# Performance work log

Measured on AMD Instinct MI355X. Metric: run time of the kernel, lower is better.

The kernel has to match this reference:

```python
import jax, jax.numpy as jnp
import numpy as np
from jax.ops import segment_sum

N_NODES = 100000
N_EDGES = 1600000
IN_DIM, HID_DIM, OUT_DIM = 64, 48, 32


def setup_inputs() -> dict:
    key = jax.random.key(0)
    ks = jax.random.split(key, 4)
    x = jax.random.normal(ks[0], (N_NODES, IN_DIM), dtype=jnp.float32)
    edge_index = jax.random.randint(ks[1], (2, N_EDGES), 0, N_NODES, dtype=jnp.int64)
    W1 = jax.random.normal(ks[2], (IN_DIM, HID_DIM), dtype=jnp.float32) / np.sqrt(IN_DIM)
    b1 = jnp.zeros((HID_DIM,), dtype=jnp.float32)
    W2 = jax.random.normal(ks[3], (HID_DIM, OUT_DIM), dtype=jnp.float32) / np.sqrt(HID_DIM)
    b2 = jnp.zeros((OUT_DIM,), dtype=jnp.float32)
    return {"x": x, "edge_index": edge_index, "W1": W1, "b1": b1, "W2": W2, "b2": b2}


def _gcn_conv(x, W, b, src, dst, deg_inv_sqrt, n_nodes):
    # GCNConv: out = D^{-1/2} (A + I) D^{-1/2} (x W) + b
    h = x @ W                                   # [N, F_out]
    norm = deg_inv_sqrt[src] * deg_inv_sqrt[dst]  # [E+N]
    msg = h[src] * norm[:, None]                # gather + scale
    out = segment_sum(msg, dst, num_segments=n_nodes)  # scatter-add over dst
    return out + b


def reference(x, edge_index, W1, b1, W2, b2):
    n = x.shape[0]
    loop = jnp.arange(n, dtype=edge_index.dtype)
    src = jnp.concatenate([edge_index[0], loop])  # add self-loops (PyG default)
    dst = jnp.concatenate([edge_index[1], loop])
    deg = segment_sum(jnp.ones_like(dst, dtype=x.dtype), dst, num_segments=n)
    deg_inv_sqrt = jnp.where(deg > 0, jax.lax.rsqrt(jnp.maximum(deg, 1.0)), 0.0)
    h = _gcn_conv(x, W1, b1, src, dst, deg_inv_sqrt, n)
    h = jax.nn.relu(h)
    embeddings = _gcn_conv(h, W2, b2, src, dst, deg_inv_sqrt, n)
    return embeddings
```

## Files before the change

### kernel.cpp

```cpp
#include <hip/hip_runtime.h>
#include <hip/hip_fp16.h>


#define NN 100000
#define NE 1600000
#define NPB 128
#define NBUCK ((NN + NPB - 1) / NPB)
#define PBITS 17
#define PMASK ((1 << PBITS) - 1)
#define CHB 3
#define CHS 14
#define NKEY (NPB << CHB)
#define PART_B 512
#define EPT 8
#define PART_G ((NE + PART_B * EPT - 1) / (PART_B * EPT))
#define CAP 4096
#define UN 8

struct alignas(8)  half4 { __half2 lo, hi; };
struct alignas(16) half8 { __half2 a, b, c, d; };

__global__ void k_part(const int* __restrict__ src, const int* __restrict__ dst,
                       int* __restrict__ cursor, int* __restrict__ packed) {
    __shared__ int h[NBUCK];
    __shared__ int base[NBUCK];
    for (int i = threadIdx.x; i < NBUCK; i += blockDim.x) h[i] = 0;
    __syncthreads();
    int ebase = blockIdx.x * (PART_B * EPT);
    for (int k = 0; k < EPT; ++k) {
        int e = ebase + k * PART_B + threadIdx.x;
        if (e < NE) atomicAdd(&h[dst[e] >> 7], 1);
    }
    __syncthreads();
    for (int i = threadIdx.x; i < NBUCK; i += blockDim.x) {
        int c = h[i];
        if (c) base[i] = atomicAdd(&cursor[i], c);
        h[i] = 0;
    }
    __syncthreads();
    for (int k = 0; k < EPT; ++k) {
        int e = ebase + k * PART_B + threadIdx.x;
        if (e < NE) {
            int d = dst[e];
            int b = d >> 7;
            int r = atomicAdd(&h[b], 1);
            packed[(size_t)b * CAP + base[b] + r] = src[e] | ((d & (NPB - 1)) << PBITS);
        }
    }
}

__global__ void k_bsort(const int* __restrict__ packed, const int* __restrict__ cursor,
                        int* __restrict__ srcsort, unsigned int* __restrict__ rowinfo,
                        float* __restrict__ dinv) {
    __shared__ int stage[CAP];
    __shared__ int cnt[NKEY];
    __shared__ int tsum[256];
    int tid = threadIdx.x, b = blockIdx.x;
    int e0 = b * CAP, sz = cursor[b];
    for (int i = tid; i < NKEY; i += 256) cnt[i] = 0;
    __syncthreads();
    for (int i = tid; i < sz; i += 256) {
        int w = packed[e0 + i];
        stage[i] = w;
        int key = ((w >> PBITS) << CHB) | ((w & PMASK) >> CHS);
        atomicAdd(&cnt[key], 1);
    }
    __syncthreads();
    int k0 = tid * 4;
    int c0 = cnt[k0], c1 = cnt[k0 + 1], c2 = cnt[k0 + 2], c3 = cnt[k0 + 3];
    int loc = c0 + c1 + c2 + c3;
    tsum[tid] = loc;
    __syncthreads();
    for (int off = 1; off < 256; off <<= 1) {
        int v = (tid >= off) ? tsum[tid - off] : 0;
        __syncthreads();
        tsum[tid] += v;
        __syncthreads();
    }
    int base = tsum[tid] - loc;
    cnt[k0]     = base;
    cnt[k0 + 1] = base + c0;
    cnt[k0 + 2] = base + c0 + c1;
    cnt[k0 + 3] = base + c0 + c1 + c2;
    __syncthreads();
    if (tid < NPB) {
        int node = b * NPB + tid;
        int rs = cnt[tid << CHB];
        int re = (tid == NPB - 1) ? sz : cnt[(tid + 1) << CHB];
        if (node < NN) {
            rowinfo[node] = ((unsigned int)(e0 + rs) << 10) | (unsigned int)(re - rs);
            dinv[node] = rsqrtf((float)(re - rs + 1));
        }
    }
    __syncthreads();
    for (int i = tid; i < sz; i += 256) {
        int w = stage[i];
        int key = ((w >> PBITS) << CHB) | ((w & PMASK) >> CHS);
        int p = atomicAdd(&cnt[key], 1);
        srcsort[e0 + p] = w & PMASK;
    }
}

template <int K, int NC, int CPT>
__global__ __launch_bounds__(256) void
k_gemm(const float* __restrict__ X, const float* __restrict__ W,
       const float* __restrict__ dinv, __half* __restrict__ Hh, int M) {
    constexpr int CG = NC / CPT;
    constexpr int MT = (256 / CG) * 2;
    constexpr int KF4 = K / 4;
    __shared__ float w[K * NC];
    int tid = threadIdx.x;
    int R0 = blockIdx.x * MT;
    for (int i = tid; i < K * NC; i += 256) w[i] = W[i];
    __syncthreads();

    int tc = tid % CG, tr = tid / CG;
    int r0 = R0 + 2 * tr, r1 = r0 + 1;
    int c0 = tc * CPT;
    bool ok0 = r0 < M, ok1 = r1 < M;
    const float4* X4 = (const float4*)X;
    const float4 z4 = make_float4(0.f, 0.f, 0.f, 0.f);

    float acc[2][CPT];
#pragma unroll
    for (int rr = 0; rr < 2; ++rr)
#pragma unroll
        for (int j = 0; j < CPT; ++j) acc[rr][j] = 0.f;

#pragma unroll 2
    for (int k4 = 0; k4 < KF4; ++k4) {
        float4 xa = ok0 ? X4[(size_t)r0 * KF4 + k4] : z4;
        float4 xb = ok1 ? X4[(size_t)r1 * KF4 + k4] : z4;
        float ar[4] = {xa.x, xa.y, xa.z, xa.w};
        float br[4] = {xb.x, xb.y, xb.z, xb.w};
#pragma unroll
        for (int j = 0; j < 4; ++j) {
            float va = ar[j], vb = br[j];
#pragma unroll
            for (int q = 0; q < CPT / 4; ++q) {
                float4 wv = *(const float4*)&w[(4 * k4 + j) * NC + c0 + 4 * q];
                acc[0][q*4+0] = fmaf(va, wv.x, acc[0][q*4+0]);
                acc[0][q*4+1] = fmaf(va, wv.y, acc[0][q*4+1]);
                acc[0][q*4+2] = fmaf(va, wv.z, acc[0][q*4+2]);
                acc[0][q*4+3] = fmaf(va, wv.w, acc[0][q*4+3]);
                acc[1][q*4+0] = fmaf(vb, wv.x, acc[1][q*4+0]);
                acc[1][q*4+1] = fmaf(vb, wv.y, acc[1][q*4+1]);
                acc[1][q*4+2] = fmaf(vb, wv.z, acc[1][q*4+2]);
                acc[1][q*4+3] = fmaf(vb, wv.w, acc[1][q*4+3]);
            }
        }
    }
#pragma unroll
    for (int rr = 0; rr < 2; ++rr) {
        int gr = r0 + rr;
        if (gr >= M) continue;
        float d = dinv[gr];
#pragma unroll
        for (int q = 0; q < CPT / 4; ++q) {
            __half2 p0 = __floats2half2_rn(acc[rr][q*4+0] * d, acc[rr][q*4+1] * d);
            __half2 p1 = __floats2half2_rn(acc[rr][q*4+2] * d, acc[rr][q*4+3] * d);
            half4 hv; hv.lo = p0; hv.hi = p1;
            *(half4*)(Hh + (size_t)gr * NC + c0 + 4 * q) = hv;
        }
    }
}

__global__ __launch_bounds__(256) void
k_fused48(const __half* __restrict__ Hh, const unsigned int* __restrict__ rowinfo,
          const int* __restrict__ srcsort, const float* __restrict__ dinv,
          const float* __restrict__ b1, const float* __restrict__ W2,
          __half* __restrict__ Hh2) {
    constexpr int ROWS = 128, XS = 49;
    __shared__ float Xs[ROWS * XS];
    __shared__ float w2[48 * 32];
    __shared__ float bb[48];
    int tid = threadIdx.x;
    int R0 = blockIdx.x * ROWS;
    for (int i = tid; i < 48 * 32; i += 256) w2[i] = W2[i];
    if (tid < 48) bb[tid] = b1[tid];
    __syncthreads();

    for (int t = tid; t < ROWS * 6; t += 256) {
        int lr = t / 6, q = t - lr * 6;
        int r = R0 + lr;
        if (r >= NN) continue;
        half8 sv = *(const half8*)(Hh + (size_t)r * 48 + 8 * q);
        float2 f0 = __half22float2(sv.a), f1 = __half22float2(sv.b);
        float2 f2 = __half22float2(sv.c), f3 = __half22float2(sv.d);
        float a0 = f0.x, a1 = f0.y, a2 = f1.x, a3 = f1.y;
        float a4 = f2.x, a5 = f2.y, a6 = f3.x, a7 = f3.y;
        unsigned int rp = rowinfo[r];
        int e0 = rp >> 10, e1 = e0 + (int)(rp & 1023);
        for (int e = e0; e < e1; e += UN) {
            int ss[UN]; float ms[UN];
#pragma unroll
            for (int u = 0; u < UN; ++u) {
                int ee = e + u;
                bool ok = ee < e1;
                ss[u] = srcsort[ok ? ee : e0];
                ms[u] = ok ? 1.f : 0.f;
            }
            half8 vv[UN];
#pragma unroll
            for (int u = 0; u < UN; ++u)
                vv[u] = *(const half8*)(Hh + (size_t)ss[u] * 48 + 8 * q);
#pragma unroll
            for (int u = 0; u < UN; ++u) {
                float2 g0 = __half22float2(vv[u].a), g1 = __half22float2(vv[u].b);
                float2 g2 = __half22float2(vv[u].c), g3 = __half22float2(vv[u].d);
                float m = ms[u];
                a0 = fmaf(g0.x, m, a0); a1 = fmaf(g0.y, m, a1);
                a2 = fmaf(g1.x, m, a2); a3 = fmaf(g1.y, m, a3);
                a4 = fmaf(g2.x, m, a4); a5 = fmaf(g2.y, m, a5);
                a6 = fmaf(g3.x, m, a6); a7 = fmaf(g3.y, m, a7);
            }
        }
        float d = dinv[r];
        float* xr = &Xs[lr * XS + 8 * q];
        const float* bf = &bb[8 * q];
        xr[0] = fmaxf(fmaf(a0, d, bf[0]), 0.f);
        xr[1] = fmaxf(fmaf(a1, d, bf[1]), 0.f);
        xr[2] = fmaxf(fmaf(a2, d, bf[2]), 0.f);
        xr[3] = fmaxf(fmaf(a3, d, bf[3]), 0.f);
        xr[4] = fmaxf(fmaf(a4, d, bf[4]), 0.f);
        xr[5] = fmaxf(fmaf(a5, d, bf[5]), 0.f);
        xr[6] = fmaxf(fmaf(a6, d, bf[6]), 0.f);
        xr[7] = fmaxf(fmaf(a7, d, bf[7]), 0.f);
    }
    __syncthreads();

    int tc = tid & 3, tr = tid >> 2;
    int r0l = 2 * tr, c0 = tc * 8;
    float acc[2][8];
#pragma unroll
    for (int rr = 0; rr < 2; ++rr)
#pragma unroll
        for (int j = 0; j < 8; ++j) acc[rr][j] = 0.f;
#pragma unroll 4
    for (int k = 0; k < 48; ++k) {
        float x0 = Xs[r0l * XS + k];
        float x1 = Xs[(r0l + 1) * XS + k];
        float4 wv0 = *(const float4*)&w2[k * 32 + c0];
        float4 wv1 = *(const float4*)&w2[k * 32 + c0 + 4];
        acc[0][0] = fmaf(x0, wv0.x, acc[0][0]); acc[0][1] = fmaf(x0, wv0.y, acc[0][1]);
        acc[0][2] = fmaf(x0, wv0.z, acc[0][2]); acc[0][3] = fmaf(x0, wv0.w, acc[0][3]);
        acc[0][4] = fmaf(x0, wv1.x, acc[0][4]); acc[0][5] = fmaf(x0, wv1.y, acc[0][5]);
        acc[0][6] = fmaf(x0, wv1.z, acc[0][6]); acc[0][7] = fmaf(x0, wv1.w, acc[0][7]);
        acc[1][0] = fmaf(x1, wv0.x, acc[1][0]); acc[1][1] = fmaf(x1, wv0.y, acc[1][1]);
        acc[1][2] = fmaf(x1, wv0.z, acc[1][2]); acc[1][3] = fmaf(x1, wv0.w, acc[1][3]);
        acc[1][4] = fmaf(x1, wv1.x, acc[1][4]); acc[1][5] = fmaf(x1, wv1.y, acc[1][5]);
        acc[1][6] = fmaf(x1, wv1.z, acc[1][6]); acc[1][7] = fmaf(x1, wv1.w, acc[1][7]);
    }
#pragma unroll
    for (int rr = 0; rr < 2; ++rr) {
        int gr = R0 + r0l + rr;
        if (gr >= NN) continue;
        float d = dinv[gr];
        __half2 p0 = __floats2half2_rn(acc[rr][0] * d, acc[rr][1] * d);
        __half2 p1 = __floats2half2_rn(acc[rr][2] * d, acc[rr][3] * d);
        __half2 p2 = __floats2half2_rn(acc[rr][4] * d, acc[rr][5] * d);
        __half2 p3 = __floats2half2_rn(acc[rr][6] * d, acc[rr][7] * d);
        half8 hv; hv.a = p0; hv.b = p1; hv.c = p2; hv.d = p3;
        *(half8*)(Hh2 + (size_t)gr * 32 + c0) = hv;
    }
}

template <int NC>
__global__ void k_agg(const __half* __restrict__ Hh, const unsigned int* __restrict__ rowinfo,
                      const int* __restrict__ srcsort, const float* __restrict__ dinv,
                      const float* __restrict__ bias, float* __restrict__ out) {
    constexpr int Q = NC / 8;
    int idx = blockIdx.x * blockDim.x + threadIdx.x;
    if (idx >= NN * Q) return;
    int r = idx / Q, q = idx - r * Q;
    half8 sv = *(const half8*)(Hh + (size_t)r * NC + 8 * q);
    float2 f0 = __half22float2(sv.a), f1 = __half22float2(sv.b);
    float2 f2 = __half22float2(sv.c), f3 = __half22float2(sv.d);
    float a0 = f0.x, a1 = f0.y, a2 = f1.x, a3 = f1.y;
    float a4 = f2.x, a5 = f2.y, a6 = f3.x, a7 = f3.y;
    unsigned int rp = rowinfo[r];
    int e0 = rp >> 10, e1 = e0 + (int)(rp & 1023);
    for (int e = e0; e < e1; e += UN) {
        int ss[UN]; float ms[UN];
#pragma unroll
        for (int u = 0; u < UN; ++u) {
            int ee = e + u;
            bool ok = ee < e1;
            ss[u] = srcsort[ok ? ee : e0];
            ms[u] = ok ? 1.f : 0.f;
        }
        half8 vv[UN];
#pragma unroll
        for (int u = 0; u < UN; ++u)
            vv[u] = *(const half8*)(Hh + (size_t)ss[u] * NC + 8 * q);
#pragma unroll
        for (int u = 0; u < UN; ++u) {
            float2 g0 = __half22float2(vv[u].a), g1 = __half22float2(vv[u].b);
            float2 g2 = __half22float2(vv[u].c), g3 = __half22float2(vv[u].d);
            float m = ms[u];
            a0 = fmaf(g0.x, m, a0); a1 = fmaf(g0.y, m, a1);
            a2 = fmaf(g1.x, m, a2); a3 = fmaf(g1.y, m, a3);
            a4 = fmaf(g2.x, m, a4); a5 = fmaf(g2.y, m, a5);
            a6 = fmaf(g3.x, m, a6); a7 = fmaf(g3.y, m, a7);
        }
    }
    float d = dinv[r];
    const float4* b4 = (const float4*)bias;
    float4 bv0 = b4[2 * q], bv1 = b4[2 * q + 1];
    a0 = fmaf(a0, d, bv0.x); a1 = fmaf(a1, d, bv0.y);
    a2 = fmaf(a2, d, bv0.z); a3 = fmaf(a3, d, bv0.w);
    a4 = fmaf(a4, d, bv1.x); a5 = fmaf(a5, d, bv1.y);
    a6 = fmaf(a6, d, bv1.z); a7 = fmaf(a7, d, bv1.w);
    float4* o4 = (float4*)(out + (size_t)r * NC + 8 * q);
    o4[0] = make_float4(a0, a1, a2, a3);
    o4[1] = make_float4(a4, a5, a6, a7);
}

extern "C" void kernel_launch(void* const* d_in, const int* in_sizes, int n_in,
                              void* d_out, int out_size, void* d_ws, size_t ws_size,
                              hipStream_t stream) {
    const float* x  = (const float*)d_in[0];
    const int*   ei = (const int*)d_in[1];
    const float* W1 = (const float*)d_in[2];
    const float* b1 = (const float*)d_in[3];
    const float* W2 = (const float*)d_in[4];
    const float* b2 = (const float*)d_in[5];
    float* out = (float*)d_out;

    const int* src = ei;
    const int* dst = ei + NE;

    char* p = (char*)d_ws;
    auto take = [&](size_t elems) { void* q = p; p += ((elems * 4 + 255) & ~255ull); return q; };
    int*          cursor  = (int*)take(NBUCK);
    unsigned int* rowinfo = (unsigned int*)take(NN);
    float*        dinv    = (float*)take(NN);
    int*          srcsort = (int*)take((size_t)NBUCK * CAP);
    __half*       Hh      = (__half*)take((size_t)NN * 24);
    int*          packed  = (int*)take((size_t)NBUCK * CAP);
    __half*       Hh2     = (__half*)packed;

    const int B = 256;
    const int GB = (NN + 127) / 128;
    hipMemsetAsync(cursor, 0, NBUCK * sizeof(int), stream);
    k_part<<<PART_G, PART_B, 0, stream>>>(src, dst, cursor, packed);
    k_bsort<<<NBUCK, 256, 0, stream>>>(packed, cursor, srcsort, rowinfo, dinv);

    k_gemm<64, 48, 12><<<GB, 256, 0, stream>>>(x, W1, dinv, Hh, NN);
    k_fused48<<<GB, 256, 0, stream>>>(Hh, rowinfo, srcsort, dinv, b1, W2, Hh2);
    k_agg<32><<<(NN * 4 + B - 1) / B, B, 0, stream>>>(Hh2, rowinfo, srcsort, dinv, b2, out);
}
```

Before: 207.0 us.

## Merge first GEMM with edge partitioning into one launch, move source scaling to gather

The layer-1 GEMM and the edge-partition pass now run in a single kernel, with block indices split between the two jobs, so that independent work overlaps and one launch is removed. Because the GEMM now runs before degrees are known, it no longer multiplies by dinv[src]. The aggregation kernel instead loads dinv for each gathered neighbour and for the self row. This adds one extra random 4-byte gather per edge in the fused layer-1 kernel and enlarges the partition blocks' shared-memory footprint by the W buffer.

```diff
diff --git a/kernel.cpp b/kernel.cpp
--- a/kernel.cpp
+++ b/kernel.cpp
@@ -11,40 +11,98 @@
 #define CHB 3
 #define CHS 14
 #define NKEY (NPB << CHB)
-#define PART_B 512
-#define EPT 8
-#define PART_G ((NE + PART_B * EPT - 1) / (PART_B * EPT))
 #define CAP 4096
 #define UN 8
+#define GEMMB ((NN + 127) / 128)
+#define EPT 8
+#define PARTB ((NE + 2047) / 2048)
 
 struct alignas(8)  half4 { __half2 lo, hi; };
 struct alignas(16) half8 { __half2 a, b, c, d; };
 
-__global__ void k_part(const int* __restrict__ src, const int* __restrict__ dst,
-                       int* __restrict__ cursor, int* __restrict__ packed) {
+__global__ __launch_bounds__(256) void
+k_fat(const float* __restrict__ X, const float* __restrict__ W,
+      __half* __restrict__ Hh,
+      const int* __restrict__ src, const int* __restrict__ dst,
+      int* __restrict__ cursor, int* __restrict__ packed) {
+    __shared__ float w[64 * 48];
     __shared__ int h[NBUCK];
     __shared__ int base[NBUCK];
-    for (int i = threadIdx.x; i < NBUCK; i += blockDim.x) h[i] = 0;
-    __syncthreads();
-    int ebase = blockIdx.x * (PART_B * EPT);
-    for (int k = 0; k < EPT; ++k) {
-        int e = ebase + k * PART_B + threadIdx.x;
-        if (e < NE) atomicAdd(&h[dst[e] >> 7], 1);
-    }
-    __syncthreads();
-    for (int i = threadIdx.x; i < NBUCK; i += blockDim.x) {
-        int c = h[i];
-        if (c) base[i] = atomicAdd(&cursor[i], c);
-        h[i] = 0;
-    }
-    __syncthreads();
-    for (int k = 0; k < EPT; ++k) {
-        int e = ebase + k * PART_B + threadIdx.x;
-        if (e < NE) {
-            int d = dst[e];
-            int b = d >> 7;
-            int r = atomicAdd(&h[b], 1);
-            packed[(size_t)b * CAP + base[b] + r] = src[e] | ((d & (NPB - 1)) << PBITS);
+    int tid = threadIdx.x;
+    if (blockIdx.x < GEMMB) {
+        int R0 = blockIdx.x * 128;
+        for (int i = tid; i < 64 * 48; i += 256) w[i] = W[i];
+        __syncthreads();
+        int tc = tid & 3, tr = tid >> 2;
+        int r0 = R0 + 2 * tr, r1 = r0 + 1;
+        int c0 = tc * 12;
+        bool ok0 = r0 < NN, ok1 = r1 < NN;
+        const float4* X4 = (const float4*)X;
+        const float4 z4 = make_float4(0.f, 0.f, 0.f, 0.f);
+        float acc[2][12];
+#pragma unroll
+        for (int rr = 0; rr < 2; ++rr)
+#pragma unroll
+            for (int j = 0; j < 12; ++j) acc[rr][j] = 0.f;
+#pragma unroll 2
+        for (int k4 = 0; k4 < 16; ++k4) {
+            float4 xa = ok0 ? X4[(size_t)r0 * 16 + k4] : z4;
+            float4 xb = ok1 ? X4[(size_t)r1 * 16 + k4] : z4;
+            float ar[4] = {xa.x, xa.y, xa.z, xa.w};
+            float br[4] = {xb.x, xb.y, xb.z, xb.w};
+#pragma unroll
+            for (int j = 0; j < 4; ++j) {
+                float va = ar[j], vb = br[j];
+#pragma unroll
+                for (int q = 0; q < 3; ++q) {
+                    float4 wv = *(const float4*)&w[(4 * k4 + j) * 48 + c0 + 4 * q];
+                    acc[0][q*4+0] = fmaf(va, wv.x, acc[0][q*4+0]);
+                    acc[0][q*4+1] = fmaf(va, wv.y, acc[0][q*4+1]);
+                    acc[0][q*4+2] = fmaf(va, wv.z, acc[0][q*4+2]);
+                    acc[0][q*4+3] = fmaf(va, wv.w, acc[0][q*4+3]);
+                    acc[1][q*4+0] = fmaf(vb, wv.x, acc[1][q*4+0]);
+                    acc[1][q*4+1] = fmaf(vb, wv.y, acc[1][q*4+1]);
+                    acc[1][q*4+2] = fmaf(vb, wv.z, acc[1][q*4+2]);
+                    acc[1][q*4+3] = fmaf(vb, wv.w, acc[1][q*4+3]);
+                }
+            }
+        }
+#pragma unroll
+        for (int rr = 0; rr < 2; ++rr) {
+            int gr = r0 + rr;
+            if (gr >= NN) continue;
+#pragma unroll
+            for (int q = 0; q < 3; ++q) {
+                __half2 p0 = __floats2half2_rn(acc[rr][q*4+0], acc[rr][q*4+1]);
+                __half2 p1 = __floats2half2_rn(acc[rr][q*4+2], acc[rr][q*4+3]);
+                half4 hv; hv.lo = p0; hv.hi = p1;
+                *(half4*)(Hh + (size_t)gr * 48 + c0 + 4 * q) = hv;
+            }
+        }
+    } else {
+        int pb = blockIdx.x - GEMMB;
+        for (int i = tid; i < NBUCK; i += 256) h[i] = 0;
+        __syncthreads();
+        int ebase = pb * 2048;
+        for (int k = 0; k < EPT; ++k) {
+            int e = ebase + k * 256 + tid;
+            if (e < NE) atomicAdd(&h[dst[e] >> 7], 1);
+        }
+        __syncthreads();
+        for (int i = tid; i < NBUCK; i += 256) {
+            int c = h[i];
+            if (c) base[i] = atomicAdd(&cursor[i], c);
+            h[i] = 0;
+        }
+        __syncthreads();
+        for (int k = 0; k < EPT; ++k) {
+            int e = ebase + k * 256 + tid;
+            if (e < NE) {
+                int d = dst[e];
+                int b = d >> 7;
+                int r = atomicAdd(&h[b], 1);
+                packed[(size_t)b * CAP + base[b] + r] = src[e] | ((d & (NPB - 1)) << PBITS);
+            }
         }
     }
 }
@@ -98,70 +156,6 @@
         int key = ((w >> PBITS) << CHB) | ((w & PMASK) >> CHS);
         int p = atomicAdd(&cnt[key], 1);
         srcsort[e0 + p] = w & PMASK;
-    }
-}
-
-template <int K, int NC, int CPT>
-__global__ __launch_bounds__(256) void
-k_gemm(const float* __restrict__ X, const float* __restrict__ W,
-       const float* __restrict__ dinv, __half* __restrict__ Hh, int M) {
-    constexpr int CG = NC / CPT;
-    constexpr int MT = (256 / CG) * 2;
-    constexpr int KF4 = K / 4;
-    __shared__ float w[K * NC];
-    int tid = threadIdx.x;
-    int R0 = blockIdx.x * MT;
-    for (int i = tid; i < K * NC; i += 256) w[i] = W[i];
-    __syncthreads();
-
-    int tc = tid % CG, tr = tid / CG;
-    int r0 = R0 + 2 * tr, r1 = r0 + 1;
-    int c0 = tc * CPT;
-    bool ok0 = r0 < M, ok1 = r1 < M;
-    const float4* X4 = (const float4*)X;
-    const float4 z4 = make_float4(0.f, 0.f, 0.f, 0.f);
-
-    float acc[2][CPT];
-#pragma unroll
-    for (int rr = 0; rr < 2; ++rr)
-#pragma unroll
-        for (int j = 0; j < CPT; ++j) acc[rr][j] = 0.f;
-
-#pragma unroll 2
-    for (int k4 = 0; k4 < KF4; ++k4) {
-        float4 xa = ok0 ? X4[(size_t)r0 * KF4 + k4] : z4;
-        float4 xb = ok1 ? X4[(size_t)r1 * KF4 + k4] : z4;
-        float ar[4] = {xa.x, xa.y, xa.z, xa.w};
-        float br[4] = {xb.x, xb.y, xb.z, xb.w};
-#pragma unroll
-        for (int j = 0; j < 4; ++j) {
-            float va = ar[j], vb = br[j];
-#pragma unroll
-            for (int q = 0; q < CPT / 4; ++q) {
-                float4 wv = *(const float4*)&w[(4 * k4 + j) * NC + c0 + 4 * q];
-                acc[0][q*4+0] = fmaf(va, wv.x, acc[0][q*4+0]);
-                acc[0][q*4+1] = fmaf(va, wv.y, acc[0][q*4+1]);
-                acc[0][q*4+2] = fmaf(va, wv.z, acc[0][q*4+2]);
-                acc[0][q*4+3] = fmaf(va, wv.w, acc[0][q*4+3]);
-                acc[1][q*4+0] = fmaf(vb, wv.x, acc[1][q*4+0]);
-                acc[1][q*4+1] = fmaf(vb, wv.y, acc[1][q*4+1]);
-                acc[1][q*4+2] = fmaf(vb, wv.z, acc[1][q*4+2]);
-                acc[1][q*4+3] = fmaf(vb, wv.w, acc[1][q*4+3]);
-            }
-        }
-    }
-#pragma unroll
-    for (int rr = 0; rr < 2; ++rr) {
-        int gr = r0 + rr;
-        if (gr >= M) continue;
-        float d = dinv[gr];
-#pragma unroll
-        for (int q = 0; q < CPT / 4; ++q) {
-            __half2 p0 = __floats2half2_rn(acc[rr][q*4+0] * d, acc[rr][q*4+1] * d);
-            __half2 p1 = __floats2half2_rn(acc[rr][q*4+2] * d, acc[rr][q*4+3] * d);
-            half4 hv; hv.lo = p0; hv.hi = p1;
-            *(half4*)(Hh + (size_t)gr * NC + c0 + 4 * q) = hv;
-        }
     }
 }
 
@@ -184,38 +178,40 @@
         int lr = t / 6, q = t - lr * 6;
         int r = R0 + lr;
         if (r >= NN) continue;
+        float d = dinv[r];
         half8 sv = *(const half8*)(Hh + (size_t)r * 48 + 8 * q);
         float2 f0 = __half22float2(sv.a), f1 = __half22float2(sv.b);
         float2 f2 = __half22float2(sv.c), f3 = __half22float2(sv.d);
-        float a0 = f0.x, a1 = f0.y, a2 = f1.x, a3 = f1.y;
-        float a4 = f2.x, a5 = f2.y, a6 = f3.x, a7 = f3.y;
+        float a0 = f0.x * d, a1 = f0.y * d, a2 = f1.x * d, a3 = f1.y * d;
+        float a4 = f2.x * d, a5 = f2.y * d, a6 = f3.x * d, a7 = f3.y * d;
         unsigned int rp = rowinfo[r];
         int e0 = rp >> 10, e1 = e0 + (int)(rp & 1023);
         for (int e = e0; e < e1; e += UN) {
-            int ss[UN]; float ms[UN];
+            int ss[UN]; bool okb[UN];
 #pragma unroll
             for (int u = 0; u < UN; ++u) {
                 int ee = e + u;
-                bool ok = ee < e1;
-                ss[u] = srcsort[ok ? ee : e0];
-                ms[u] = ok ? 1.f : 0.f;
-            }
+                okb[u] = ee < e1;
+                ss[u] = srcsort[okb[u] ? ee : e0];
+            }
+            float dd[UN];
+#pragma unroll
+            for (int u = 0; u < UN; ++u) dd[u] = dinv[ss[u]];
             half8 vv[UN];
 #pragma unroll
             for (int u = 0; u < UN; ++u)
                 vv[u] = *(const half8*)(Hh + (size_t)ss[u] * 48 + 8 * q);
 #pragma unroll
             for (int u = 0; u < UN; ++u) {
+                float m = okb[u] ? dd[u] : 0.f;
                 float2 g0 = __half22float2(vv[u].a), g1 = __half22float2(vv[u].b);
                 float2 g2 = __half22float2(vv[u].c), g3 = __half22float2(vv[u].d);
-                float m = ms[u];
                 a0 = fmaf(g0.x, m, a0); a1 = fmaf(g0.y, m, a1);
                 a2 = fmaf(g1.x, m, a2); a3 = fmaf(g1.y, m, a3);
                 a4 = fmaf(g2.x, m, a4); a5 = fmaf(g2.y, m, a5);
                 a6 = fmaf(g3.x, m, a6); a7 = fmaf(g3.y, m, a7);
             }
         }
-        float d = dinv[r];
         float* xr = &Xs[lr * XS + 8 * q];
         const float* bf = &bb[8 * q];
         xr[0] = fmaxf(fmaf(a0, d, bf[0]), 0.f);
@@ -341,12 +337,10 @@
     __half*       Hh2     = (__half*)packed;
 
     const int B = 256;
-    const int GB = (NN + 127) / 128;
+    const int GB = GEMMB;
     hipMemsetAsync(cursor, 0, NBUCK * sizeof(int), stream);
-    k_part<<<PART_G, PART_B, 0, stream>>>(src, dst, cursor, packed);
+    k_fat<<<GEMMB + PARTB, 256, 0, stream>>>(x, W1, Hh, src, dst, cursor, packed);
     k_bsort<<<NBUCK, 256, 0, stream>>>(packed, cursor, srcsort, rowinfo, dinv);
-
-    k_gemm<64, 48, 12><<<GB, 256, 0, stream>>>(x, W1, dinv, Hh, NN);
     k_fused48<<<GB, 256, 0, stream>>>(Hh, rowinfo, srcsort, dinv, b1, W2, Hh2);
     k_agg<32><<<(NN * 4 + B - 1) / B, B, 0, stream>>>(Hh2, rowinfo, srcsort, dinv, b2, out);
 }
```

Result: no change. 210.4 us (+1.6%).
